# Kernel tuning notes

Hardware: AMD Instinct MI355X
Metric: run time of the kernel (lower is better)

## Reference

```python
import jax, jax.numpy as jnp
import numpy as np

LORA_DIM = 16          # hard-coded in module
LORA_TOKEN_INDEX = 1   # lora_dim*layer_sequence + 1 with layer_sequence=0
B, S, D, H = 4, 2048, 1024, 4096  # num_hiddens = 4*num_input (forced by view())


def setup_inputs() -> dict:
    key = jax.random.key(0)
    ks = jax.random.split(key, 6)
    x = jax.random.normal(ks[0], (B, S, D), dtype=jnp.float32)
    W1 = jax.random.normal(ks[1], (H, D), dtype=jnp.float32) * 0.02
    b1 = jnp.zeros((H,), dtype=jnp.float32)
    W2 = jax.random.normal(ks[2], (D, H), dtype=jnp.float32) * 0.02
    b2 = jnp.zeros((D,), dtype=jnp.float32)
    scale = jnp.asarray(0.001, dtype=jnp.float32)  # nn.Parameter(torch.tensor(0.001))
    return {"x": x, "W1": W1, "b1": b1, "W2": W2, "b2": b2, "scale": scale}


def reference(x, W1, b1, W2, b2, scale):
    Bx, Sx, Dx = x.shape
    Hx = W1.shape[0]  # = 4*Dx
    # 16 lora tokens starting at LORA_TOKEN_INDEX
    lt = jax.lax.dynamic_slice_in_dim(x, LORA_TOKEN_INDEX, LORA_DIM, axis=1)
    even = lt[:, ::2, :]  # (B, 8, D)
    odd = lt[:, 1::2, :]  # (B, 8, D)
    # per-sample low-rank weight updates:
    # result_multiplication[b,k] = outer(even[b,k], odd[b,k]) (D,D)
    # matrix1 = first 4 blocks stacked -> (B, 4D, D); matrix2 = last 4 reshaped -> (B, D, 4D)
    m1 = (even[:, :4, :, None] * odd[:, :4, None, :]).reshape(Bx, Hx, Dx)
    m2 = (even[:, 4:, :, None] * odd[:, 4:, None, :]).reshape(Bx, Dx, Hx)
    # x @ (W1 + scale*m1)^T + b1, fused without repeating W1 per batch
    h = jnp.einsum('bsd,hd->bsh', x, W1) + scale * jnp.einsum('bsd,bhd->bsh', x, m1) + b1
    h = jax.nn.gelu(h, approximate=False)  # torch nn.GELU default = exact erf
    out = jnp.einsum('bsh,oh->bso', h, W2) + scale * jnp.einsum('bsh,boh->bso', h, m2) + b2
    return out
```

## Files before the change

kernel.cpp:

```cpp
#include <hip/hip_runtime.h>
#include <cstdint>
#include <cstddef>

#define MROWS 8192
#define DDIM  1024
#define HDIM  4096

typedef __bf16 bf16x8 __attribute__((ext_vector_type(8)));
typedef float  f32x4  __attribute__((ext_vector_type(4)));

typedef __attribute__((address_space(1))) void* as1_vp;
typedef __attribute__((address_space(3))) void* as3_vp;

__device__ __forceinline__ unsigned short f2bf(float f) {
  unsigned int u = __builtin_bit_cast(unsigned int, f);
  u += 0x7fffu + ((u >> 16) & 1u);
  return (unsigned short)(u >> 16);
}
__device__ __forceinline__ float bf2f(unsigned short h) {
  return __builtin_bit_cast(float, (unsigned int)h << 16);
}

__device__ __forceinline__ float fast_gelu(float x) {
  float x3 = x * x * x;
  float z = 0.7978845608028654f * x + 0.03567740814f * x3;
  float e = __builtin_amdgcn_exp2f(z * 2.8853900817779268f);
  float t = 1.0f - 2.0f * __builtin_amdgcn_rcpf(e + 1.0f);
  return 0.5f * x * (1.0f + t);
}

__device__ __forceinline__ void gld_lds16(const unsigned short* g, unsigned short* lds) {
  __builtin_amdgcn_global_load_lds((as1_vp)(uintptr_t)g, (as3_vp)lds, 16, 0, 0);
}

__global__ __launch_bounds__(256) void cvt2_kernel(
    const float* __restrict__ w1, const float* __restrict__ w2,
    unsigned short* __restrict__ w1b, unsigned short* __restrict__ w2b) {
  int i = blockIdx.x * 256 + threadIdx.x;
  const float* src; unsigned short* dst; int off;
  if (i < 1048576) { src = w1; dst = w1b; off = i; }
  else             { src = w2; dst = w2b; off = i - 1048576; }
  float4 v = ((const float4*)src)[off];
  ushort4 o;
  o.x = f2bf(v.x); o.y = f2bf(v.y); o.z = f2bf(v.z); o.w = f2bf(v.w);
  ((ushort4*)dst)[off] = o;
}

__global__ __launch_bounds__(256) void p1_kernel(const float* __restrict__ x,
                                                 float* __restrict__ p1,
                                                 unsigned short* __restrict__ xb) {
  const int wave = threadIdx.x >> 6, lane = threadIdx.x & 63;
  const int m = blockIdx.x * 4 + wave;
  const int b = m >> 11;
  const float4* xrow4 = (const float4*)(x + (size_t)m * DDIM);
  const float4* od4   = (const float4*)(x + ((size_t)b * 2048 + 2) * DDIM);
  ushort4* xbrow4 = (ushort4*)(xb + (size_t)m * DDIM);
  float a0 = 0.f, a1 = 0.f, a2 = 0.f, a3 = 0.f;
#pragma unroll
  for (int it = 0; it < 4; ++it) {
    int g = it * 64 + lane;
    float4 v = xrow4[g];
    ushort4 o; o.x = f2bf(v.x); o.y = f2bf(v.y); o.z = f2bf(v.z); o.w = f2bf(v.w);
    xbrow4[g] = o;
    float4 o0 = od4[g];
    float4 o1 = od4[512 + g];
    float4 o2 = od4[1024 + g];
    float4 o3 = od4[1536 + g];
    a0 += v.x * o0.x + v.y * o0.y + v.z * o0.z + v.w * o0.w;
    a1 += v.x * o1.x + v.y * o1.y + v.z * o1.z + v.w * o1.w;
    a2 += v.x * o2.x + v.y * o2.y + v.z * o2.z + v.w * o2.w;
    a3 += v.x * o3.x + v.y * o3.y + v.z * o3.z + v.w * o3.w;
  }
#pragma unroll
  for (int off = 32; off > 0; off >>= 1) {
    a0 += __shfl_down(a0, off);
    a1 += __shfl_down(a1, off);
    a2 += __shfl_down(a2, off);
    a3 += __shfl_down(a3, off);
  }
  if (lane == 0) {
    float4 r; r.x = a0; r.y = a1; r.z = a2; r.w = a3;
    ((float4*)p1)[m] = r;
  }
}

__global__ __launch_bounds__(256) void p2_kernel(const unsigned short* __restrict__ hact,
                                                 const float* __restrict__ x,
                                                 float* __restrict__ p2) {
  const int wave = threadIdx.x >> 6, lane = threadIdx.x & 63;
  const int m = blockIdx.x * 4 + wave;
  const int b = m >> 11;
  const ushort4* hrow4 = (const ushort4*)(hact + (size_t)m * HDIM);
  const float4* od4    = (const float4*)(x + ((size_t)b * 2048 + 10) * DDIM);
  float acc[4][4] = {{0.f}};
#pragma unroll
  for (int it = 0; it < 4; ++it) {
    int g = it * 64 + lane;
    float h[4][4];
#pragma unroll
    for (int r = 0; r < 4; ++r) {
      ushort4 hv = hrow4[r * 256 + g];
      h[r][0] = bf2f(hv.x); h[r][1] = bf2f(hv.y); h[r][2] = bf2f(hv.z); h[r][3] = bf2f(hv.w);
    }
#pragma unroll
    for (int i = 0; i < 4; ++i) {
      float4 ov = od4[i * 512 + g];
#pragma unroll
      for (int r = 0; r < 4; ++r)
        acc[i][r] += ov.x * h[r][0] + ov.y * h[r][1] + ov.z * h[r][2] + ov.w * h[r][3];
    }
  }
#pragma unroll
  for (int i = 0; i < 4; ++i)
#pragma unroll
    for (int r = 0; r < 4; ++r)
#pragma unroll
      for (int off = 32; off > 0; off >>= 1)
        acc[i][r] += __shfl_down(acc[i][r], off);
  if (lane == 0) {
#pragma unroll
    for (int i = 0; i < 4; ++i) {
      float4 v; v.x = acc[i][0]; v.y = acc[i][1]; v.z = acc[i][2]; v.w = acc[i][3];
      ((float4*)(p2 + (size_t)m * 16))[i] = v;
    }
  }
}

__device__ __forceinline__ void gemm_bt_tile(const unsigned short* __restrict__ A,
                                             const unsigned short* __restrict__ B,
                                             const int K, const int m0, const int n0,
                                             unsigned short* As, unsigned short* Bs,
                                             f32x4 acc[4][4]) {
  const int tid  = threadIdx.x;
  const int wave = tid >> 6;
  const int lane = tid & 63;
  const int quad = lane >> 4;
  const int l16  = lane & 15;
  const int wm   = (wave >> 1) * 64;
  const int wn   = (wave & 1) * 64;

  const unsigned short* ga[4]; const unsigned short* gb[4];
#pragma unroll
  for (int s = 0; s < 4; ++s) {
    int idx = wave * 256 + s * 64 + lane;
    int r = idx >> 3, sl = idx & 7;
    int c = (sl - r) & 7;
    ga[s] = A + (size_t)(m0 + r) * K + c * 8;
    gb[s] = B + (size_t)(n0 + r) * K + c * 8;
  }

  for (int k0 = 0; k0 < K; k0 += 64) {
    __syncthreads();
#pragma unroll
    for (int s = 0; s < 4; ++s) gld_lds16(ga[s] + k0, As + (wave * 4 + s) * 512);
#pragma unroll
    for (int s = 0; s < 4; ++s) gld_lds16(gb[s] + k0, Bs + (wave * 4 + s) * 512);
    __syncthreads();
#pragma unroll
    for (int kk = 0; kk < 64; kk += 32) {
      bf16x8 a[4], b[4];
      const int cbase = (kk >> 3) + quad;
#pragma unroll
      for (int i = 0; i < 4; ++i) {
        const int ra = wm + i * 16 + l16;
        const int rb = wn + i * 16 + l16;
        a[i] = *(const bf16x8*)(As + ra * 64 + ((cbase + ra) & 7) * 8);
        b[i] = *(const bf16x8*)(Bs + rb * 64 + ((cbase + rb) & 7) * 8);
      }
#pragma unroll
      for (int i = 0; i < 4; ++i)
#pragma unroll
        for (int j = 0; j < 4; ++j)
          acc[i][j] = __builtin_amdgcn_mfma_f32_16x16x32_bf16(a[i], b[j], acc[i][j], 0, 0, 0);
    }
  }
}

__global__ __launch_bounds__(256) void gemm1_kernel(
    const unsigned short* __restrict__ xb, const unsigned short* __restrict__ w1b,
    const float* __restrict__ x, const float* __restrict__ b1,
    const float* __restrict__ p1, const float* __restrict__ scale_p,
    unsigned short* __restrict__ hact) {
  __shared__ __align__(16) unsigned short As[128 * 64];
  __shared__ __align__(16) unsigned short Bs[128 * 64];
  const int n0 = blockIdx.x * 128;
  const int m0 = blockIdx.y * 128;
  f32x4 acc[4][4];
  const f32x4 z = {0.f, 0.f, 0.f, 0.f};
#pragma unroll
  for (int i = 0; i < 4; ++i)
#pragma unroll
    for (int j = 0; j < 4; ++j) acc[i][j] = z;

  gemm_bt_tile(xb, w1b, DDIM, m0, n0, As, Bs, acc);

  const int tid = threadIdx.x;
  const int wave = tid >> 6, lane = tid & 63, quad = lane >> 4, l16 = lane & 15;
  const int wm = (wave >> 1) * 64, wn = (wave & 1) * 64;
  const float sc = scale_p[0];
  const int bidx = m0 >> 11;
  const int i1 = (n0 + wn) >> 10;
  const float* exrow = x + ((size_t)(bidx * 2048 + 1 + 2 * i1)) * DDIM;

  float exv[4], b1v[4]; int nn[4];
#pragma unroll
  for (int j = 0; j < 4; ++j) {
    nn[j]  = n0 + wn + j * 16 + l16;
    exv[j] = exrow[nn[j] & 1023];
    b1v[j] = b1[nn[j]];
  }
#pragma unroll
  for (int i = 0; i < 4; ++i) {
#pragma unroll
    for (int r = 0; r < 4; ++r) {
      const int m = m0 + wm + i * 16 + quad * 4 + r;
      const float pv = p1[(size_t)m * 4 + i1] * sc;
#pragma unroll
      for (int j = 0; j < 4; ++j) {
        float v = acc[i][j][r] + b1v[j] + pv * exv[j];
        hact[(size_t)m * HDIM + nn[j]] = f2bf(fast_gelu(v));
      }
    }
  }
}

__global__ __launch_bounds__(256) void gemm2_kernel(
    const unsigned short* __restrict__ hact, const unsigned short* __restrict__ w2b,
    const float* __restrict__ x, const float* __restrict__ b2,
    const float* __restrict__ p2, const float* __restrict__ scale_p,
    float* __restrict__ out) {
  __shared__ __align__(16) unsigned short As[128 * 64];
  __shared__ __align__(16) unsigned short Bs[128 * 64];
  const int n0 = blockIdx.x * 128;
  const int m0 = blockIdx.y * 128;
  f32x4 acc[4][4];
  const f32x4 z = {0.f, 0.f, 0.f, 0.f};
#pragma unroll
  for (int i = 0; i < 4; ++i)
#pragma unroll
    for (int j = 0; j < 4; ++j) acc[i][j] = z;

  gemm_bt_tile(hact, w2b, HDIM, m0, n0, As, Bs, acc);

  const int tid = threadIdx.x;
  const int wave = tid >> 6, lane = tid & 63, quad = lane >> 4, l16 = lane & 15;
  const int wm = (wave >> 1) * 64, wn = (wave & 1) * 64;
  const float sc = scale_p[0];
  const int bidx = m0 >> 11;
  const int i2 = (n0 + wn) >> 8;
  const float* evrow = x + ((size_t)(bidx * 2048 + 9 + 2 * i2)) * DDIM;

  float4 ev[4]; float b2v[4]; int nn[4];
#pragma unroll
  for (int j = 0; j < 4; ++j) {
    nn[j] = n0 + wn + j * 16 + l16;
    const int q = nn[j] & 255;
    ev[j]  = *(const float4*)(evrow + 4 * q);
    b2v[j] = b2[nn[j]];
  }
#pragma unroll
  for (int i = 0; i < 4; ++i) {
#pragma unroll
    for (int r = 0; r < 4; ++r) {
      const int m = m0 + wm + i * 16 + quad * 4 + r;
      const float4 pv = *(const float4*)(p2 + (size_t)m * 16 + i2 * 4);
#pragma unroll
      for (int j = 0; j < 4; ++j) {
        float lora = ev[j].x * pv.x + ev[j].y * pv.y + ev[j].z * pv.z + ev[j].w * pv.w;
        out[(size_t)m * DDIM + nn[j]] = acc[i][j][r] + b2v[j] + sc * lora;
      }
    }
  }
}

extern "C" void kernel_launch(void* const* d_in, const int* in_sizes, int n_in,
                              void* d_out, int out_size, void* d_ws, size_t ws_size,
                              hipStream_t stream) {
  const float* x     = (const float*)d_in[0];
  const float* W1    = (const float*)d_in[1];
  const float* b1    = (const float*)d_in[2];
  const float* W2    = (const float*)d_in[3];
  const float* b2    = (const float*)d_in[4];
  const float* scale = (const float*)d_in[5];
  float* out = (float*)d_out;

  char* ws = (char*)d_ws;
  unsigned short* xb   = (unsigned short*)(ws);
  unsigned short* w1b  = (unsigned short*)(ws + 16777216);
  unsigned short* w2b  = (unsigned short*)(ws + 25165824);
  unsigned short* hact = (unsigned short*)(ws + 33554432);
  float*          p1   = (float*)(ws + 100663296);
  float*          p2   = (float*)(ws + 100794368);

  cvt2_kernel<<<dim3(8192), dim3(256), 0, stream>>>(W1, W2, w1b, w2b);
  p1_kernel<<<dim3(MROWS / 4), dim3(256), 0, stream>>>(x, p1, xb);
  gemm1_kernel<<<dim3(HDIM / 128, MROWS / 128), dim3(256), 0, stream>>>(xb, w1b, x, b1, p1, scale, hact);
  p2_kernel<<<dim3(MROWS / 4), dim3(256), 0, stream>>>(hact, x, p2);
  gemm2_kernel<<<dim3(DDIM / 128, MROWS / 128), dim3(256), 0, stream>>>(hact, w2b, x, b2, p2, scale, out);
}
```

Before: 289.7 us.

## Split-K gemm2 with atomic accumulation and merge small prep kernels

Merges the weight-conversion and p1 kernels into one launch, and the p2 kernel with a zero-fill of the output into another. gemm2 is split along K into two halves over a z-grid dimension, and each half accumulates into the output with float atomics. Only the first half adds the bias and LoRA terms. The aim is to double the block count for gemm2, which otherwise has only 512 tiles, and to cut launch overhead, at the cost of extra atomic traffic, a zero-fill pass and nondeterministic summation order.

```diff
diff --git a/kernel.cpp b/kernel.cpp
--- a/kernel.cpp
+++ b/kernel.cpp
@@ -33,24 +33,25 @@
   __builtin_amdgcn_global_load_lds((as1_vp)(uintptr_t)g, (as3_vp)lds, 16, 0, 0);
 }
 
-__global__ __launch_bounds__(256) void cvt2_kernel(
-    const float* __restrict__ w1, const float* __restrict__ w2,
-    unsigned short* __restrict__ w1b, unsigned short* __restrict__ w2b) {
-  int i = blockIdx.x * 256 + threadIdx.x;
-  const float* src; unsigned short* dst; int off;
-  if (i < 1048576) { src = w1; dst = w1b; off = i; }
-  else             { src = w2; dst = w2b; off = i - 1048576; }
-  float4 v = ((const float4*)src)[off];
-  ushort4 o;
-  o.x = f2bf(v.x); o.y = f2bf(v.y); o.z = f2bf(v.z); o.w = f2bf(v.w);
-  ((ushort4*)dst)[off] = o;
-}
-
-__global__ __launch_bounds__(256) void p1_kernel(const float* __restrict__ x,
-                                                 float* __restrict__ p1,
-                                                 unsigned short* __restrict__ xb) {
+__global__ __launch_bounds__(256) void pre_kernel(
+    const float* __restrict__ x, const float* __restrict__ w1,
+    const float* __restrict__ w2, unsigned short* __restrict__ xb,
+    unsigned short* __restrict__ w1b, unsigned short* __restrict__ w2b,
+    float* __restrict__ p1) {
+  if (blockIdx.x < 8192) {
+    int i = blockIdx.x * 256 + threadIdx.x;
+    const float* src; unsigned short* dst; int off;
+    if (i < 1048576) { src = w1; dst = w1b; off = i; }
+    else             { src = w2; dst = w2b; off = i - 1048576; }
+    float4 v = ((const float4*)src)[off];
+    ushort4 o;
+    o.x = f2bf(v.x); o.y = f2bf(v.y); o.z = f2bf(v.z); o.w = f2bf(v.w);
+    ((ushort4*)dst)[off] = o;
+    return;
+  }
+  const int bid = blockIdx.x - 8192;
   const int wave = threadIdx.x >> 6, lane = threadIdx.x & 63;
-  const int m = blockIdx.x * 4 + wave;
+  const int m = bid * 4 + wave;
   const int b = m >> 11;
   const float4* xrow4 = (const float4*)(x + (size_t)m * DDIM);
   const float4* od4   = (const float4*)(x + ((size_t)b * 2048 + 2) * DDIM);
@@ -84,9 +85,15 @@
   }
 }
 
-__global__ __launch_bounds__(256) void p2_kernel(const unsigned short* __restrict__ hact,
-                                                 const float* __restrict__ x,
-                                                 float* __restrict__ p2) {
+__global__ __launch_bounds__(256) void mid_kernel(
+    const unsigned short* __restrict__ hact, const float* __restrict__ x,
+    float* __restrict__ p2, float* __restrict__ out) {
+  if (blockIdx.x >= 2048) {
+    int i = (blockIdx.x - 2048) * 256 + threadIdx.x;
+    float4 z; z.x = 0.f; z.y = 0.f; z.z = 0.f; z.w = 0.f;
+    ((float4*)out)[i] = z;
+    return;
+  }
   const int wave = threadIdx.x >> 6, lane = threadIdx.x & 63;
   const int m = blockIdx.x * 4 + wave;
   const int b = m >> 11;
@@ -128,7 +135,8 @@
 
 __device__ __forceinline__ void gemm_bt_tile(const unsigned short* __restrict__ A,
                                              const unsigned short* __restrict__ B,
-                                             const int K, const int m0, const int n0,
+                                             const int ld, const int Kloop,
+                                             const int m0, const int n0,
                                              unsigned short* As, unsigned short* Bs,
                                              f32x4 acc[4][4]) {
   const int tid  = threadIdx.x;
@@ -145,11 +153,11 @@
     int idx = wave * 256 + s * 64 + lane;
     int r = idx >> 3, sl = idx & 7;
     int c = (sl - r) & 7;
-    ga[s] = A + (size_t)(m0 + r) * K + c * 8;
-    gb[s] = B + (size_t)(n0 + r) * K + c * 8;
-  }
-
-  for (int k0 = 0; k0 < K; k0 += 64) {
+    ga[s] = A + (size_t)(m0 + r) * ld + c * 8;
+    gb[s] = B + (size_t)(n0 + r) * ld + c * 8;
+  }
+
+  for (int k0 = 0; k0 < Kloop; k0 += 64) {
     __syncthreads();
 #pragma unroll
     for (int s = 0; s < 4; ++s) gld_lds16(ga[s] + k0, As + (wave * 4 + s) * 512);
@@ -192,7 +200,7 @@
 #pragma unroll
     for (int j = 0; j < 4; ++j) acc[i][j] = z;
 
-  gemm_bt_tile(xb, w1b, DDIM, m0, n0, As, Bs, acc);
+  gemm_bt_tile(xb, w1b, DDIM, DDIM, m0, n0, As, Bs, acc);
 
   const int tid = threadIdx.x;
   const int wave = tid >> 6, lane = tid & 63, quad = lane >> 4, l16 = lane & 15;
@@ -233,6 +241,7 @@
   __shared__ __align__(16) unsigned short Bs[128 * 64];
   const int n0 = blockIdx.x * 128;
   const int m0 = blockIdx.y * 128;
+  const int kz = blockIdx.z;
   f32x4 acc[4][4];
   const f32x4 z = {0.f, 0.f, 0.f, 0.f};
 #pragma unroll
@@ -240,34 +249,48 @@
 #pragma unroll
     for (int j = 0; j < 4; ++j) acc[i][j] = z;
 
-  gemm_bt_tile(hact, w2b, HDIM, m0, n0, As, Bs, acc);
+  gemm_bt_tile(hact + kz * 2048, w2b + kz * 2048, HDIM, 2048, m0, n0, As, Bs, acc);
 
   const int tid = threadIdx.x;
   const int wave = tid >> 6, lane = tid & 63, quad = lane >> 4, l16 = lane & 15;
   const int wm = (wave >> 1) * 64, wn = (wave & 1) * 64;
-  const float sc = scale_p[0];
-  const int bidx = m0 >> 11;
-  const int i2 = (n0 + wn) >> 8;
-  const float* evrow = x + ((size_t)(bidx * 2048 + 9 + 2 * i2)) * DDIM;
-
-  float4 ev[4]; float b2v[4]; int nn[4];
-#pragma unroll
-  for (int j = 0; j < 4; ++j) {
-    nn[j] = n0 + wn + j * 16 + l16;
-    const int q = nn[j] & 255;
-    ev[j]  = *(const float4*)(evrow + 4 * q);
-    b2v[j] = b2[nn[j]];
-  }
-#pragma unroll
-  for (int i = 0; i < 4; ++i) {
-#pragma unroll
-    for (int r = 0; r < 4; ++r) {
-      const int m = m0 + wm + i * 16 + quad * 4 + r;
-      const float4 pv = *(const float4*)(p2 + (size_t)m * 16 + i2 * 4);
-#pragma unroll
-      for (int j = 0; j < 4; ++j) {
-        float lora = ev[j].x * pv.x + ev[j].y * pv.y + ev[j].z * pv.z + ev[j].w * pv.w;
-        out[(size_t)m * DDIM + nn[j]] = acc[i][j][r] + b2v[j] + sc * lora;
+  int nn[4];
+#pragma unroll
+  for (int j = 0; j < 4; ++j) nn[j] = n0 + wn + j * 16 + l16;
+
+  if (kz == 0) {
+    const float sc = scale_p[0];
+    const int bidx = m0 >> 11;
+    const int i2 = (n0 + wn) >> 8;
+    const float* evrow = x + ((size_t)(bidx * 2048 + 9 + 2 * i2)) * DDIM;
+    float4 ev[4]; float b2v[4];
+#pragma unroll
+    for (int j = 0; j < 4; ++j) {
+      ev[j]  = *(const float4*)(evrow + 4 * (nn[j] & 255));
+      b2v[j] = b2[nn[j]];
+    }
+#pragma unroll
+    for (int i = 0; i < 4; ++i) {
+#pragma unroll
+      for (int r = 0; r < 4; ++r) {
+        const int m = m0 + wm + i * 16 + quad * 4 + r;
+        const float4 pv = *(const float4*)(p2 + (size_t)m * 16 + i2 * 4);
+#pragma unroll
+        for (int j = 0; j < 4; ++j) {
+          float lora = ev[j].x * pv.x + ev[j].y * pv.y + ev[j].z * pv.z + ev[j].w * pv.w;
+          atomicAdd(&out[(size_t)m * DDIM + nn[j]], acc[i][j][r] + b2v[j] + sc * lora);
+        }
+      }
+    }
+  } else {
+#pragma unroll
+    for (int i = 0; i < 4; ++i) {
+#pragma unroll
+      for (int r = 0; r < 4; ++r) {
+        const int m = m0 + wm + i * 16 + quad * 4 + r;
+#pragma unroll
+        for (int j = 0; j < 4; ++j)
+          atomicAdd(&out[(size_t)m * DDIM + nn[j]], acc[i][j][r]);
       }
     }
   }
@@ -292,9 +315,8 @@
   float*          p1   = (float*)(ws + 100663296);
   float*          p2   = (float*)(ws + 100794368);
 
-  cvt2_kernel<<<dim3(8192), dim3(256), 0, stream>>>(W1, W2, w1b, w2b);
-  p1_kernel<<<dim3(MROWS / 4), dim3(256), 0, stream>>>(x, p1, xb);
+  pre_kernel<<<dim3(10240), dim3(256), 0, stream>>>(x, W1, W2, xb, w1b, w2b, p1);
   gemm1_kernel<<<dim3(HDIM / 128, MROWS / 128), dim3(256), 0, stream>>>(xb, w1b, x, b1, p1, scale, hact);
-  p2_kernel<<<dim3(MROWS / 4), dim3(256), 0, stream>>>(hact, x, p2);
-  gemm2_kernel<<<dim3(DDIM / 128, MROWS / 128), dim3(256), 0, stream>>>(hact, w2b, x, b2, p2, scale, out);
-}
+  mid_kernel<<<dim3(10240), dim3(256), 0, stream>>>(hact, x, p2, out);
+  gemm2_kernel<<<dim3(DDIM / 128, MROWS / 128, 2), dim3(256), 0, stream>>>(hact, w2b, x, b2, p2, scale, out);
+}
```

Result: slower. 336.1 us (+16.0%).
